# Optimization experiments

Measured on AMD Instinct MI355X. Metric: run time of the kernel, lower is better.

Reference implementation:

```python
import jax, jax.numpy as jnp
import numpy as np

N_NODES = 100000
NNZ = 3200000
D_FEAT = 128


def setup_inputs() -> dict:
    key = jax.random.key(0)
    k1, k2, k3 = jax.random.split(key, 3)
    indices = jax.random.randint(k1, (2, NNZ), 0, N_NODES, dtype=jnp.int64 if jax.config.jax_enable_x64 else jnp.int32)
    values = jax.random.normal(k2, (NNZ,), dtype=jnp.float32)
    b = jax.random.normal(k3, (N_NODES, D_FEAT), dtype=jnp.float32)
    return {"indices": indices, "values": values, "n_rows": N_NODES, "b": b}


def reference(indices, values, n_rows, b):
    # out = sparse_coo(indices, values, [n_rows, n_rows]) @ b
    # out[i] = sum_{e: row[e]==i} values[e] * b[col[e]]
    row, col = indices[0], indices[1]
    gathered = values[:, None] * b[col]              # [nnz, d]
    out = jax.ops.segment_sum(gathered, row, num_segments=n_rows)  # [n_rows, d]
    return out
```

## Files before the change

kernel.cpp:

```cpp
#include <hip/hip_runtime.h>


#define D_FEAT 128
#define NB_FINE_MAX 2048
#define NSUP_MAX 128
#define CHUNK_A 6144
#define BCAP 4608
#define QSPLIT 8
#define STG_CAP 3072
#define NT 16
#define CT_SHIFT 13
#define NKEY 1024

__device__ __forceinline__ unsigned short f2bf(float f) {
    unsigned u = __float_as_uint(f);
    u += 0x7FFFu + ((u >> 16) & 1u);
    return (unsigned short)(u >> 16);
}
__device__ __forceinline__ float bf2f(unsigned short h) {
    return __uint_as_float((unsigned)h << 16);
}

__global__ void spmm_atomic_kernel(const int* __restrict__ rowidx,
                                   const int* __restrict__ colidx,
                                   const float* __restrict__ vals,
                                   const float* __restrict__ b,
                                   float* __restrict__ out, int nnz) {
    int gtid = blockIdx.x * blockDim.x + threadIdx.x;
    int group = gtid >> 5, fid = gtid & 31;
    int ngroup = (gridDim.x * blockDim.x) >> 5;
    for (int e = group; e < nnz; e += ngroup) {
        int r = rowidx[e], c = colidx[e];
        float v = vals[e];
        float4 bv = reinterpret_cast<const float4*>(b + (size_t)c * D_FEAT)[fid];
        float* orow = out + (size_t)r * D_FEAT + (size_t)fid * 4;
        atomicAdd(orow + 0, v * bv.x);
        atomicAdd(orow + 1, v * bv.y);
        atomicAdd(orow + 2, v * bv.z);
        atomicAdd(orow + 3, v * bv.w);
    }
}

__global__ void bconv_kernel(const float* __restrict__ bmat,
                             ushort* __restrict__ b16, int n4) {
    int i = blockIdx.x * blockDim.x + threadIdx.x;
    int gs = gridDim.x * blockDim.x;
    for (int k = i; k < n4; k += gs) {
        float4 v = reinterpret_cast<const float4*>(bmat)[k];
        ushort4 o;
        o.x = f2bf(v.x); o.y = f2bf(v.y); o.z = f2bf(v.z); o.w = f2bf(v.w);
        reinterpret_cast<ushort4*>(b16)[k] = o;
    }
}

__global__ void histAB_kernel(const int* __restrict__ rowidx,
                              int* __restrict__ histB, int* __restrict__ histA,
                              int nnz) {
    __shared__ int lcnt[NB_FINE_MAX];
    for (int i = threadIdx.x; i < NB_FINE_MAX; i += blockDim.x) lcnt[i] = 0;
    __syncthreads();
    int gid = blockIdx.x * blockDim.x + threadIdx.x;
    int gsz = gridDim.x * blockDim.x;
    for (int e = gid; e < nnz; e += gsz)
        atomicAdd(&lcnt[rowidx[e] >> 6], 1);
    __syncthreads();
    for (int i = threadIdx.x; i < NB_FINE_MAX; i += blockDim.x)
        if (lcnt[i]) atomicAdd(&histB[i], lcnt[i]);
    for (int sa = threadIdx.x; sa < NSUP_MAX; sa += blockDim.x) {
        int s = 0;
        for (int k = 0; k < 16; ++k) s += lcnt[sa * 16 + k];
        if (s) atomicAdd(&histA[sa], s);
    }
}

__global__ void scanAB_kernel(const int* __restrict__ histB, const int* __restrict__ histA,
                              int* __restrict__ gbaseB, int* __restrict__ gcurB,
                              int* __restrict__ gbaseA, int* __restrict__ gcurA) {
    __shared__ int hs[1024];
    int t = threadIdx.x;
    int c0 = histB[2 * t], c1 = histB[2 * t + 1];
    hs[t] = c0 + c1;
    __syncthreads();
    for (int off = 1; off < 1024; off <<= 1) {
        int u = (t >= off) ? hs[t - off] : 0;
        __syncthreads();
        hs[t] += u;
        __syncthreads();
    }
    int excl = hs[t] - (c0 + c1);
    gbaseB[2 * t] = excl;          gcurB[2 * t] = excl;
    gbaseB[2 * t + 1] = excl + c0; gcurB[2 * t + 1] = excl + c0;
    __syncthreads();
    int vA = (t < NSUP_MAX) ? histA[t] : 0;
    if (t < NSUP_MAX) hs[t] = vA;
    __syncthreads();
    for (int off = 1; off < NSUP_MAX; off <<= 1) {
        int u = (t < NSUP_MAX && t >= off) ? hs[t - off] : 0;
        __syncthreads();
        if (t < NSUP_MAX) hs[t] += u;
        __syncthreads();
    }
    if (t < NSUP_MAX) {
        int eA = hs[t] - vA;
        gbaseA[t] = eA; gcurA[t] = eA;
    }
}

__global__ __launch_bounds__(512)
void passA_kernel(const int* __restrict__ rowidx, const int* __restrict__ colidx,
                  const float* __restrict__ vals, int* __restrict__ gcurA,
                  float2* __restrict__ cvA, int nnz) {
    __shared__ float2 stage[CHUNK_A];
    __shared__ unsigned char bsel[CHUNK_A];
    __shared__ int loff[NSUP_MAX], cur[NSUP_MAX], gpos[NSUP_MAX], sc[NSUP_MAX];
    int t = threadIdx.x;
    int chunk = (nnz + gridDim.x - 1) / gridDim.x;
    int beg = blockIdx.x * chunk;
    int end = min(beg + chunk, nnz);
    int n = end - beg;
    if (n <= 0) return;

    for (int i = t; i < NSUP_MAX; i += 512) loff[i] = 0;
    __syncthreads();
    for (int e = beg + t; e < end; e += 512)
        atomicAdd(&loff[rowidx[e] >> 10], 1);
    __syncthreads();
    int v = (t < NSUP_MAX) ? loff[t] : 0;
    if (t < NSUP_MAX) sc[t] = v;
    __syncthreads();
    for (int off = 1; off < NSUP_MAX; off <<= 1) {
        int u = (t < NSUP_MAX && t >= off) ? sc[t - off] : 0;
        __syncthreads();
        if (t < NSUP_MAX) sc[t] += u;
        __syncthreads();
    }
    if (t < NSUP_MAX) { loff[t] = sc[t] - v; cur[t] = sc[t] - v; }
    __syncthreads();
    for (int e = beg + t; e < end; e += 512) {
        int r = rowidx[e];
        int sb = r >> 10;
        int pos = atomicAdd(&cur[sb], 1);
        stage[pos] = make_float2(__int_as_float(((r & 1023) << 17) | colidx[e]), vals[e]);
        bsel[pos] = (unsigned char)sb;
    }
    __syncthreads();
    if (t < NSUP_MAX) {
        int cnt = cur[t] - loff[t];
        if (cnt > 0) gpos[t] = atomicAdd(&gcurA[t], cnt);
    }
    __syncthreads();
    for (int i = t; i < n; i += 512) {
        int sb = bsel[i];
        cvA[gpos[sb] + (i - loff[sb])] = stage[i];
    }
}

__global__ __launch_bounds__(512)
void passB_kernel(const int* __restrict__ gbaseA, const int* __restrict__ gendA,
                  const float2* __restrict__ cvA, int* __restrict__ gcurB,
                  float2* __restrict__ cv) {
    __shared__ float2 stage[BCAP];
    __shared__ unsigned char fsel[BCAP];
    __shared__ int cnt16[16], gpos16[16], cur16[16];
    int t = threadIdx.x;
    int s = blockIdx.x / QSPLIT, q = blockIdx.x % QSPLIT;
    int sb = gbaseA[s], se = gendA[s];
    int ns = se - sb;
    if (ns <= 0) return;
    int qlen = (ns + QSPLIT - 1) / QSPLIT;
    int qb = sb + q * qlen;
    int qe = min(qb + qlen, se);
    for (int rb = qb; rb < qe; rb += BCAP) {
        int m = min(BCAP, qe - rb);
        if (t < 16) cnt16[t] = 0;
        __syncthreads();
        for (int i = t; i < m; i += 512) {
            float2 p = cvA[rb + i];
            stage[i] = p;
            int fl = (__float_as_int(p.x) >> 17) >> 6;
            fsel[i] = (unsigned char)fl;
            atomicAdd(&cnt16[fl], 1);
        }
        __syncthreads();
        if (t == 0) {
            for (int i = 0; i < 16; ++i) {
                int c = cnt16[i];
                cur16[i] = 0;
                if (c > 0) gpos16[i] = atomicAdd(&gcurB[s * 16 + i], c);
            }
        }
        __syncthreads();
        for (int i = t; i < m; i += 512) {
            float2 p = stage[i];
            int fl = fsel[i];
            int pos = atomicAdd(&cur16[fl], 1);
            int pk = __float_as_int(p.x);
            int p2 = (((pk >> 17) & 63) << 17) | (pk & 0x1FFFF);
            cv[gpos16[fl] + pos] = make_float2(__int_as_float(p2), p.y);
        }
        __syncthreads();
    }
}

#define ACCADD(P, PK, U)                                                      \
    {                                                                         \
        float cx_ = (P).y * bf2f((U).x);                                      \
        float cy_ = (P).y * bf2f((U).y);                                      \
        int kk_ = __builtin_amdgcn_readfirstlane(((PK) >> 17) & 7);           \
        switch (kk_) {                                                        \
            case 0: acc0.x += cx_; acc0.y += cy_; break;                      \
            case 1: acc1.x += cx_; acc1.y += cy_; break;                      \
            case 2: acc2.x += cx_; acc2.y += cy_; break;                      \
            case 3: acc3.x += cx_; acc3.y += cy_; break;                      \
            case 4: acc4.x += cx_; acc4.y += cy_; break;                      \
            case 5: acc5.x += cx_; acc5.y += cy_; break;                      \
            case 6: acc6.x += cx_; acc6.y += cy_; break;                      \
            default: acc7.x += cx_; acc7.y += cy_; break;                     \
        }                                                                     \
    }

__global__ __launch_bounds__(512)
void fusedmm_kernel(const int* __restrict__ gbaseB, const int* __restrict__ gendB,
                    const float2* __restrict__ cv, const ushort* __restrict__ b16,
                    float* __restrict__ out, int n_rows) {
    __shared__ float2 stg[STG_CAP];
    __shared__ int cnt[NKEY];
    __shared__ int strt[NKEY + 1];
    int* sc = (int*)stg;

    int t = threadIdx.x, bkt = blockIdx.x;
    int gb = gbaseB[bkt], ge = gendB[bkt];
    int n = ge - gb;
    int w = t >> 6, lane = t & 63;
    int rl0 = w * 8;
    const ushort2* bp = reinterpret_cast<const ushort2*>(b16) + lane;

    float2 acc0 = {0.f, 0.f}, acc1 = {0.f, 0.f}, acc2 = {0.f, 0.f}, acc3 = {0.f, 0.f};
    float2 acc4 = {0.f, 0.f}, acc5 = {0.f, 0.f}, acc6 = {0.f, 0.f}, acc7 = {0.f, 0.f};

    if (n > STG_CAP) {
        for (int j = gb; j < ge; ++j) {
            float2 p = cv[j];
            int pk = __float_as_int(p.x);
            if (((pk >> 17) >> 3) == w) {
                ushort2 u = bp[(size_t)(pk & 0x1FFFF) << 6];
                ACCADD(p, pk, u);
            }
        }
    } else {
        for (int i = t; i < NKEY; i += 512) cnt[i] = 0;
        __syncthreads();
        for (int i = t; i < n; i += 512) {
            int pk = __float_as_int(cv[gb + i].x);
            int key = (((pk & 0x1FFFF) >> CT_SHIFT) << 6) | (pk >> 17);
            atomicAdd(&cnt[key], 1);
        }
        __syncthreads();
        int c0 = cnt[2 * t], c1 = cnt[2 * t + 1];
        sc[t] = c0 + c1;
        __syncthreads();
        for (int off = 1; off < 512; off <<= 1) {
            int u = (t >= off) ? sc[t - off] : 0;
            __syncthreads();
            sc[t] += u;
            __syncthreads();
        }
        int excl = sc[t] - (c0 + c1);
        __syncthreads();
        strt[2 * t] = excl;          cnt[2 * t] = excl;
        strt[2 * t + 1] = excl + c0; cnt[2 * t + 1] = excl + c0;
        if (t == 0) strt[NKEY] = n;
        __syncthreads();
        for (int i = t; i < n; i += 512) {
            float2 p = cv[gb + i];
            int pk = __float_as_int(p.x);
            int key = (((pk & 0x1FFFF) >> CT_SHIFT) << 6) | (pk >> 17);
            int pos = atomicAdd(&cnt[key], 1);
            stg[pos] = p;
        }
        __syncthreads();
        for (int tt = 0; tt < NT; ++tt) {
            int jb = strt[(tt << 6) + rl0];
            int je = strt[(tt << 6) + rl0 + 8];
            int j = jb;
            for (; j + 7 < je; j += 8) {
                float2 p0 = stg[j],     p1 = stg[j + 1];
                float2 p2 = stg[j + 2], p3 = stg[j + 3];
                float2 p4 = stg[j + 4], p5 = stg[j + 5];
                float2 p6 = stg[j + 6], p7 = stg[j + 7];
                int k0 = __float_as_int(p0.x), k1 = __float_as_int(p1.x);
                int k2 = __float_as_int(p2.x), k3 = __float_as_int(p3.x);
                int k4 = __float_as_int(p4.x), k5 = __float_as_int(p5.x);
                int k6 = __float_as_int(p6.x), k7 = __float_as_int(p7.x);
                ushort2 u0 = bp[(size_t)(k0 & 0x1FFFF) << 6];
                ushort2 u1 = bp[(size_t)(k1 & 0x1FFFF) << 6];
                ushort2 u2 = bp[(size_t)(k2 & 0x1FFFF) << 6];
                ushort2 u3 = bp[(size_t)(k3 & 0x1FFFF) << 6];
                ushort2 u4 = bp[(size_t)(k4 & 0x1FFFF) << 6];
                ushort2 u5 = bp[(size_t)(k5 & 0x1FFFF) << 6];
                ushort2 u6 = bp[(size_t)(k6 & 0x1FFFF) << 6];
                ushort2 u7 = bp[(size_t)(k7 & 0x1FFFF) << 6];
                ACCADD(p0, k0, u0); ACCADD(p1, k1, u1);
                ACCADD(p2, k2, u2); ACCADD(p3, k3, u3);
                ACCADD(p4, k4, u4); ACCADD(p5, k5, u5);
                ACCADD(p6, k6, u6); ACCADD(p7, k7, u7);
            }
            for (; j < je; ++j) {
                float2 p = stg[j];
                int pk = __float_as_int(p.x);
                ushort2 u = bp[(size_t)(pk & 0x1FFFF) << 6];
                ACCADD(p, pk, u);
            }
        }
    }
    int rowbase = bkt * 64 + rl0;
    float2* op = reinterpret_cast<float2*>(out) + lane;
    if (rowbase + 0 < n_rows) op[(size_t)(rowbase + 0) * 64] = acc0;
    if (rowbase + 1 < n_rows) op[(size_t)(rowbase + 1) * 64] = acc1;
    if (rowbase + 2 < n_rows) op[(size_t)(rowbase + 2) * 64] = acc2;
    if (rowbase + 3 < n_rows) op[(size_t)(rowbase + 3) * 64] = acc3;
    if (rowbase + 4 < n_rows) op[(size_t)(rowbase + 4) * 64] = acc4;
    if (rowbase + 5 < n_rows) op[(size_t)(rowbase + 5) * 64] = acc5;
    if (rowbase + 6 < n_rows) op[(size_t)(rowbase + 6) * 64] = acc6;
    if (rowbase + 7 < n_rows) op[(size_t)(rowbase + 7) * 64] = acc7;
}

extern "C" void kernel_launch(void* const* d_in, const int* in_sizes, int n_in,
                              void* d_out, int out_size, void* d_ws, size_t ws_size,
                              hipStream_t stream) {
    const int*   indices = (const int*)d_in[0];
    const float* values  = (const float*)d_in[1];
    const float* b       = (const float*)d_in[3];
    float*       out     = (float*)d_out;

    const int nnz    = in_sizes[1];
    const int n_rows = out_size / D_FEAT;
    const int nbB    = (n_rows + 63) >> 6;
    const int nsup   = (n_rows + 1023) >> 10;
    const int* rowidx = indices;
    const int* colidx = indices + nnz;

    int* histB  = (int*)d_ws;
    int* histA  = histB + NB_FINE_MAX;
    int* gbaseA = histA + NSUP_MAX;
    int* gcurA  = gbaseA + NSUP_MAX;
    int* gbaseB = gcurA + NSUP_MAX;
    int* gcurB  = gbaseB + NB_FINE_MAX;
    size_t off = (size_t)(3 * NB_FINE_MAX + 3 * NSUP_MAX) * sizeof(int);
    off = (off + 255) & ~(size_t)255;
    size_t b16_bytes = ((size_t)n_rows * D_FEAT * 2 + 255) & ~(size_t)255;
    ushort* b16 = (ushort*)((char*)d_ws + off);
    float2* cv  = (float2*)((char*)d_ws + off + b16_bytes);
    float2* cvA = (float2*)d_out;

    size_t need = off + b16_bytes + (size_t)nnz * sizeof(float2);
    if (need > ws_size || (size_t)nnz * sizeof(float2) > (size_t)out_size * 4 ||
        n_rows > 131072) {
        hipMemsetAsync(d_out, 0, (size_t)out_size * sizeof(float), stream);
        spmm_atomic_kernel<<<8192, 256, 0, stream>>>(rowidx, colidx, values, b, out, nnz);
        return;
    }

    hipMemsetAsync(histB, 0, (NB_FINE_MAX + NSUP_MAX) * sizeof(int), stream);
    bconv_kernel<<<1024, 256, 0, stream>>>(b, b16, n_rows * D_FEAT / 4);
    histAB_kernel<<<512, 256, 0, stream>>>(rowidx, histB, histA, nnz);
    scanAB_kernel<<<1, 1024, 0, stream>>>(histB, histA, gbaseB, gcurB, gbaseA, gcurA);
    int gridA = (nnz + CHUNK_A - 1) / CHUNK_A;
    passA_kernel<<<gridA, 512, 0, stream>>>(rowidx, colidx, values, gcurA, cvA, nnz);
    passB_kernel<<<nsup * QSPLIT, 512, 0, stream>>>(gbaseA, gcurA, cvA, gcurB, cv);
    fusedmm_kernel<<<nbB, 512, 0, stream>>>(gbaseB, gcurB, cv, b16, out, n_rows);
}
```

Before: 288.1 us.

## Split each 64-row bucket across two blocks in fused SpMM kernel

Launches two blocks per 64-row bucket, each handling 32 rows (4 per wavefront), so the grid doubles and each block accumulates only half the rows. Each block still scans the whole bucket's entries to filter its half, which doubles reads of the bucket's cv data, but it cuts per-block staging and key counts and reduces accumulator registers. The aim is more parallelism and occupancy for the gather-heavy SpMM at the cost of the redundant filtering pass.

```diff
diff --git a/kernel.cpp b/kernel.cpp
--- a/kernel.cpp
+++ b/kernel.cpp
@@ -7,10 +7,10 @@
 #define CHUNK_A 6144
 #define BCAP 4608
 #define QSPLIT 8
-#define STG_CAP 3072
+#define STG_CAP 2048
 #define NT 16
 #define CT_SHIFT 13
-#define NKEY 1024
+#define NKEY 512
 
 __device__ __forceinline__ unsigned short f2bf(float f) {
     unsigned u = __float_as_uint(f);
@@ -202,20 +202,16 @@
     }
 }
 
-#define ACCADD(P, PK, U)                                                      \
+#define ACCADD4(P, PK, U)                                                     \
     {                                                                         \
         float cx_ = (P).y * bf2f((U).x);                                      \
         float cy_ = (P).y * bf2f((U).y);                                      \
-        int kk_ = __builtin_amdgcn_readfirstlane(((PK) >> 17) & 7);           \
+        int kk_ = __builtin_amdgcn_readfirstlane(((PK) >> 17) & 3);           \
         switch (kk_) {                                                        \
             case 0: acc0.x += cx_; acc0.y += cy_; break;                      \
             case 1: acc1.x += cx_; acc1.y += cy_; break;                      \
             case 2: acc2.x += cx_; acc2.y += cy_; break;                      \
-            case 3: acc3.x += cx_; acc3.y += cy_; break;                      \
-            case 4: acc4.x += cx_; acc4.y += cy_; break;                      \
-            case 5: acc5.x += cx_; acc5.y += cy_; break;                      \
-            case 6: acc6.x += cx_; acc6.y += cy_; break;                      \
-            default: acc7.x += cx_; acc7.y += cy_; break;                     \
+            default: acc3.x += cx_; acc3.y += cy_; break;                     \
         }                                                                     \
     }
 
@@ -228,60 +224,69 @@
     __shared__ int strt[NKEY + 1];
     int* sc = (int*)stg;
 
-    int t = threadIdx.x, bkt = blockIdx.x;
+    int t = threadIdx.x;
+    int bkt = blockIdx.x >> 1, half = blockIdx.x & 1;
     int gb = gbaseB[bkt], ge = gendB[bkt];
-    int n = ge - gb;
     int w = t >> 6, lane = t & 63;
-    int rl0 = w * 8;
+    int r5base = w * 4;
     const ushort2* bp = reinterpret_cast<const ushort2*>(b16) + lane;
 
-    float2 acc0 = {0.f, 0.f}, acc1 = {0.f, 0.f}, acc2 = {0.f, 0.f}, acc3 = {0.f, 0.f};
-    float2 acc4 = {0.f, 0.f}, acc5 = {0.f, 0.f}, acc6 = {0.f, 0.f}, acc7 = {0.f, 0.f};
-
-    if (n > STG_CAP) {
+    float2 acc0 = {0.f, 0.f}, acc1 = {0.f, 0.f};
+    float2 acc2 = {0.f, 0.f}, acc3 = {0.f, 0.f};
+
+    for (int i = t; i < NKEY; i += 512) cnt[i] = 0;
+    __syncthreads();
+    for (int i = gb + t; i < ge; i += 512) {
+        int pk = __float_as_int(cv[i].x);
+        int rl = pk >> 17;
+        if ((rl >> 5) == half) {
+            int key = (((pk & 0x1FFFF) >> CT_SHIFT) << 5) | (rl & 31);
+            atomicAdd(&cnt[key], 1);
+        }
+    }
+    __syncthreads();
+    int v = cnt[t];
+    sc[t] = v;
+    __syncthreads();
+    for (int off = 1; off < 512; off <<= 1) {
+        int u = (t >= off) ? sc[t - off] : 0;
+        __syncthreads();
+        sc[t] += u;
+        __syncthreads();
+    }
+    int incl = sc[t];
+    __syncthreads();
+    strt[t] = incl - v;
+    cnt[t] = incl - v;
+    if (t == 511) strt[NKEY] = incl;
+    __syncthreads();
+    int nh = strt[NKEY];
+
+    if (nh > STG_CAP) {
         for (int j = gb; j < ge; ++j) {
             float2 p = cv[j];
             int pk = __float_as_int(p.x);
-            if (((pk >> 17) >> 3) == w) {
+            int rl = pk >> 17;
+            if ((rl >> 5) == half && ((rl & 31) >> 2) == w) {
                 ushort2 u = bp[(size_t)(pk & 0x1FFFF) << 6];
-                ACCADD(p, pk, u);
+                ACCADD4(p, pk, u);
             }
         }
     } else {
-        for (int i = t; i < NKEY; i += 512) cnt[i] = 0;
-        __syncthreads();
-        for (int i = t; i < n; i += 512) {
-            int pk = __float_as_int(cv[gb + i].x);
-            int key = (((pk & 0x1FFFF) >> CT_SHIFT) << 6) | (pk >> 17);
-            atomicAdd(&cnt[key], 1);
-        }
-        __syncthreads();
-        int c0 = cnt[2 * t], c1 = cnt[2 * t + 1];
-        sc[t] = c0 + c1;
-        __syncthreads();
-        for (int off = 1; off < 512; off <<= 1) {
-            int u = (t >= off) ? sc[t - off] : 0;
-            __syncthreads();
-            sc[t] += u;
-            __syncthreads();
-        }
-        int excl = sc[t] - (c0 + c1);
-        __syncthreads();
-        strt[2 * t] = excl;          cnt[2 * t] = excl;
-        strt[2 * t + 1] = excl + c0; cnt[2 * t + 1] = excl + c0;
-        if (t == 0) strt[NKEY] = n;
-        __syncthreads();
-        for (int i = t; i < n; i += 512) {
-            float2 p = cv[gb + i];
+        for (int i = gb + t; i < ge; i += 512) {
+            float2 p = cv[i];
             int pk = __float_as_int(p.x);
-            int key = (((pk & 0x1FFFF) >> CT_SHIFT) << 6) | (pk >> 17);
-            int pos = atomicAdd(&cnt[key], 1);
-            stg[pos] = p;
+            int rl = pk >> 17;
+            if ((rl >> 5) == half) {
+                int key = (((pk & 0x1FFFF) >> CT_SHIFT) << 5) | (rl & 31);
+                int pos = atomicAdd(&cnt[key], 1);
+                stg[pos] = p;
+            }
         }
         __syncthreads();
         for (int tt = 0; tt < NT; ++tt) {
-            int jb = strt[(tt << 6) + rl0];
-            int je = strt[(tt << 6) + rl0 + 8];
+            int jb = strt[(tt << 5) + r5base];
+            int je = strt[(tt << 5) + r5base + 4];
             int j = jb;
             for (; j + 7 < je; j += 8) {
                 float2 p0 = stg[j],     p1 = stg[j + 1];
@@ -300,29 +305,25 @@
                 ushort2 u5 = bp[(size_t)(k5 & 0x1FFFF) << 6];
                 ushort2 u6 = bp[(size_t)(k6 & 0x1FFFF) << 6];
                 ushort2 u7 = bp[(size_t)(k7 & 0x1FFFF) << 6];
-                ACCADD(p0, k0, u0); ACCADD(p1, k1, u1);
-                ACCADD(p2, k2, u2); ACCADD(p3, k3, u3);
-                ACCADD(p4, k4, u4); ACCADD(p5, k5, u5);
-                ACCADD(p6, k6, u6); ACCADD(p7, k7, u7);
+                ACCADD4(p0, k0, u0); ACCADD4(p1, k1, u1);
+                ACCADD4(p2, k2, u2); ACCADD4(p3, k3, u3);
+                ACCADD4(p4, k4, u4); ACCADD4(p5, k5, u5);
+                ACCADD4(p6, k6, u6); ACCADD4(p7, k7, u7);
             }
             for (; j < je; ++j) {
                 float2 p = stg[j];
                 int pk = __float_as_int(p.x);
                 ushort2 u = bp[(size_t)(pk & 0x1FFFF) << 6];
-                ACCADD(p, pk, u);
-            }
-        }
-    }
-    int rowbase = bkt * 64 + rl0;
+                ACCADD4(p, pk, u);
+            }
+        }
+    }
+    int rowbase = bkt * 64 + half * 32 + r5base;
     float2* op = reinterpret_cast<float2*>(out) + lane;
     if (rowbase + 0 < n_rows) op[(size_t)(rowbase + 0) * 64] = acc0;
     if (rowbase + 1 < n_rows) op[(size_t)(rowbase + 1) * 64] = acc1;
     if (rowbase + 2 < n_rows) op[(size_t)(rowbase + 2) * 64] = acc2;
     if (rowbase + 3 < n_rows) op[(size_t)(rowbase + 3) * 64] = acc3;
-    if (rowbase + 4 < n_rows) op[(size_t)(rowbase + 4) * 64] = acc4;
-    if (rowbase + 5 < n_rows) op[(size_t)(rowbase + 5) * 64] = acc5;
-    if (rowbase + 6 < n_rows) op[(size_t)(rowbase + 6) * 64] = acc6;
-    if (rowbase + 7 < n_rows) op[(size_t)(rowbase + 7) * 64] = acc7;
 }
 
 extern "C" void kernel_launch(void* const* d_in, const int* in_sizes, int n_in,
@@ -368,5 +369,5 @@
     int gridA = (nnz + CHUNK_A - 1) / CHUNK_A;
     passA_kernel<<<gridA, 512, 0, stream>>>(rowidx, colidx, values, gcurA, cvA, nnz);
     passB_kernel<<<nsup * QSPLIT, 512, 0, stream>>>(gbaseA, gcurA, cvA, gcurB, cv);
-    fusedmm_kernel<<<nbB, 512, 0, stream>>>(gbaseB, gcurB, cv, b16, out, n_rows);
-}
+    fusedmm_kernel<<<nbB * 2, 512, 0, stream>>>(gbaseB, gcurB, cv, b16, out, n_rows);
+}
```

Measured after the change: 267.0 us. 1.08x faster.
